# Kernel optimization log

Measured on AMD Instinct MI355X. Metric: run time of the kernel, lower is better.

The kernel has to match this reference:

```python
import jax, jax.numpy as jnp
import numpy as np
from jax import lax

LB, UB = 0.0, 0.1
N_ITERS = 32  # fixed-point iterations for water-filling rebalance


def _conv(x, w, b):
    y = lax.conv_general_dilated(x, w, (1, 1), ((1, 1), (1, 1)),
                                 dimension_numbers=("NCHW", "OIHW", "NCHW"))
    return y + b[None, :, None, None]


def _maxpool2(x):
    return lax.reduce_window(x, -jnp.inf, lax.max, (1, 1, 2, 2), (1, 1, 2, 2), "VALID")


def _linear(x, w, b):
    return x @ w.T + b


def _gru(x_num, W_ih, W_hh, b_ih, b_hh):
    # x_num: [B, S, N]; torch GRU gate order r, z, n
    B = x_num.shape[0]
    H = W_hh.shape[1]
    xs = jnp.swapaxes(x_num, 0, 1)  # [S, B, N]

    def step(h, x_t):
        gi = x_t @ W_ih.T + b_ih            # [B, 3H]
        gh = h @ W_hh.T + b_hh              # [B, 3H]
        i_r, i_z, i_n = jnp.split(gi, 3, axis=-1)
        h_r, h_z, h_n = jnp.split(gh, 3, axis=-1)
        r = jax.nn.sigmoid(i_r + h_r)
        z = jax.nn.sigmoid(i_z + h_z)
        n = jnp.tanh(i_n + r * h_n)
        h_new = (1.0 - z) * n + z * h
        return h_new, None

    h0 = jnp.zeros((B, H), dtype=x_num.dtype)
    h_last, _ = lax.scan(step, h0, xs)
    return h_last


def _rebalance_one(w):
    # vectorized fixed-point version of the per-sample while-loop water-filling
    def body(carry, _):
        old, wc = carry
        leftover = jnp.sum(old - wc)
        mask = wc != UB
        s = jnp.sum(jnp.where(mask, wc, 0.0))
        gift = jnp.where(mask & (s > 0), leftover * wc / jnp.where(s > 0, s, 1.0), 0.0)
        new_old = wc + gift
        new_wc = jnp.clip(new_old, LB, UB)
        return (new_old, new_wc), None

    init = (w, jnp.clip(w, LB, UB))
    (_, wc), _ = lax.scan(body, init, None, length=N_ITERS)
    return wc


def setup_inputs() -> dict:
    key = jax.random.key(0)
    ks = jax.random.split(key, 16)
    B, S, N, H_IMG, W_IMG, HID = 16, 60, 50, 64, 60, 128
    fc_in = 64 * (H_IMG // 4) * (W_IMG // 4)  # 15360
    sc = 0.05
    return {
        "x_num": jax.random.normal(ks[0], (B, S, N), jnp.float32),
        "x_img": jax.random.uniform(ks[1], (B, N, H_IMG, W_IMG), jnp.float32),
        "conv1_w": jax.random.normal(ks[2], (32, 1, 3, 3), jnp.float32) * sc,
        "conv1_b": jnp.zeros((32,), jnp.float32),
        "conv2_w": jax.random.normal(ks[3], (64, 32, 3, 3), jnp.float32) * sc,
        "conv2_b": jnp.zeros((64,), jnp.float32),
        "fc1_w": jax.random.normal(ks[4], (64, fc_in), jnp.float32) * 0.01,
        "fc1_b": jnp.zeros((64,), jnp.float32),
        "fc_binary_w": jax.random.normal(ks[5], (1, 64), jnp.float32) * sc,
        "fc_binary_b": jnp.zeros((1,), jnp.float32),
        "fc2_w": jax.random.normal(ks[6], (128, 64), jnp.float32) * sc,
        "fc2_b": jnp.zeros((128,), jnp.float32),
        "W_ih": jax.random.normal(ks[7], (3 * HID, N), jnp.float32) * sc,
        "W_hh": jax.random.normal(ks[8], (3 * HID, HID), jnp.float32) * sc,
        "b_ih": jnp.zeros((3 * HID,), jnp.float32),
        "b_hh": jnp.zeros((3 * HID,), jnp.float32),
        "gru_fc_w": jax.random.normal(ks[9], (N, HID), jnp.float32) * sc,
        "gru_fc_b": jnp.zeros((N,), jnp.float32),
        "fusion_w": jax.random.normal(ks[10], (64, N + 128), jnp.float32) * sc,
        "fusion_b": jnp.zeros((64,), jnp.float32),
        "final_w": jax.random.normal(ks[11], (N, 64), jnp.float32) * sc,
        "final_b": jnp.zeros((N,), jnp.float32),
    }


def reference(x_num, x_img, conv1_w, conv1_b, conv2_w, conv2_b, fc1_w, fc1_b,
              fc_binary_w, fc_binary_b, fc2_w, fc2_b, W_ih, W_hh, b_ih, b_hh,
              gru_fc_w, gru_fc_b, fusion_w, fusion_b, final_w, final_b):
    B, S, N = x_num.shape
    # GRU branch: last hidden -> Linear -> [B, N]
    h_last = _gru(x_num, W_ih, W_hh, b_ih, b_hh)
    numerical_features = _linear(h_last, gru_fc_w, gru_fc_b)

    # CNN branch on per-stock chart images
    xi = x_img.reshape(B * N, 1, x_img.shape[2], x_img.shape[3])
    h = _maxpool2(jax.nn.relu(_conv(xi, conv1_w, conv1_b)))
    h = _maxpool2(jax.nn.relu(_conv(h, conv2_w, conv2_b)))
    h = h.reshape(B * N, -1)
    feats = jax.nn.relu(_linear(h, fc1_w, fc1_b))
    binary_pred = jax.nn.sigmoid(_linear(feats, fc_binary_w, fc_binary_b))
    cnn_features = _linear(feats, fc2_w, fc2_b).reshape(B, N, -1).mean(axis=1)

    fused = jax.nn.relu(_linear(jnp.concatenate([numerical_features, cnn_features], axis=1), fusion_w, fusion_b))
    w = jax.nn.softmax(_linear(fused, final_w, final_b), axis=1)
    portfolio_weights = jax.vmap(_rebalance_one)(w)
    return portfolio_weights, binary_pred.reshape(B, N)
```

## Files before the change

### kernel.cpp

```cpp
#include <hip/hip_runtime.h>
#include <hip/hip_bf16.h>

typedef unsigned short ushort_t;
typedef short short8_t __attribute__((ext_vector_type(8)));
typedef float f32x4 __attribute__((ext_vector_type(4)));
typedef float f32x16 __attribute__((ext_vector_type(16)));
typedef ushort_t us4_t __attribute__((ext_vector_type(4)));

#define NBATCH 16
#define SEQ    60
#define NSTK   50
#define HID    128
#define G3     384
#define NIMG   800
#define IH     64
#define IW     60
#define P1H    32
#define P1W    30
#define P2C    64
#define FCIN   15360

#define OFF_WHHF   0u
#define OFF_WPREP  24576u
#define OFF_WFC1   33792u
#define OFF_GI     525312u
#define OFF_HLAST  893952u
#define OFF_POOL2  896000u
#define OFF_FC2O   7040000u
#define OFF_PART   7142400u
#define WS_FLOATS  7961600u

#define E_WHH  49152
#define E_WPR  18432
#define E_FC1  983040
#define E_TOT  (E_WHH + E_WPR + E_FC1)

struct __align__(16) ConvS {
    ushort_t pool1t[18][4][32][8];
    union {
        float    imgp[35][60];
        ushort_t pool2s[64][120];
    } u;
};
struct __align__(16) GruS {
    float    gh[16 * 388];
    ushort_t hb[16 * 136];
};
#define SMEM_BYTES 52224

__device__ __forceinline__ float fast_sig(float x) {
    const float e = __expf(-x);
    return __builtin_amdgcn_rcpf(1.f + e);
}
__device__ __forceinline__ float fast_tanh(float x) {
    const float xc = fmaxf(fminf(x, 15.f), -15.f);
    const float e = __expf(2.f * xc);
    return (e - 1.f) * __builtin_amdgcn_rcpf(e + 1.f);
}

__global__ __launch_bounds__(384) void k_pre(const float* __restrict__ xnum,
                                             const float* __restrict__ wih,
                                             const float* __restrict__ bih,
                                             const float* __restrict__ whh,
                                             const float* __restrict__ c2w,
                                             const float* __restrict__ fc1w,
                                             float* __restrict__ GI,
                                             ushort_t* __restrict__ whhf,
                                             ushort_t* __restrict__ wprep,
                                             ushort_t* __restrict__ wfc1)
{
    const int bid = blockIdx.x;
    if (bid < 960) {
        const int s = bid >> 4, b = bid & 15;
        const int j = threadIdx.x;
        const float* xr = xnum + (size_t)(b * SEQ + s) * NSTK;
        const float* wr = wih + (size_t)j * NSTK;
        float a = bih[j];
        #pragma unroll 10
        for (int k = 0; k < NSTK; ++k) a = fmaf(xr[k], wr[k], a);
        GI[((size_t)s * 16 + b) * G3 + j] = a;
        return;
    }
    const int idx = (bid - 960) * 384 + threadIdx.x;
    if (idx < E_WHH) {
        const int e = idx;
        const int i = e & 7, l = (e >> 3) & 63, ksj = e >> 9;
        const int ks = ksj & 3, jt = ksj >> 2;
        const int j = jt * 16 + (l & 15);
        const int k = ks * 32 + ((l >> 4) << 3) + i;
        __hip_bfloat16 hv = __float2bfloat16(whh[j * HID + k]);
        whhf[e] = *(ushort_t*)&hv;
    } else if (idx < E_WHH + E_WPR) {
        const int e = idx - E_WHH;
        const int i = e & 7, l = (e >> 3) & 63, rest = e >> 9;
        const int ks = rest & 1, mt = rest >> 1;
        const int tap = mt % 9, mm = mt / 9;
        const int oc = mm * 32 + (l & 31);
        const int ic = ks * 16 + ((l >> 5) << 3) + i;
        __hip_bfloat16 hv = __float2bfloat16(c2w[((size_t)oc * 32 + ic) * 9 + tap]);
        wprep[e] = *(ushort_t*)&hv;
    } else if (idx < E_TOT) {
        const int e = idx - (E_WHH + E_WPR);
        const int i = e & 7, l = (e >> 3) & 63, rest = e >> 9;
        const int n = rest & 3, T = rest >> 2;
        const int oc = n * 16 + (l & 15);
        const int k = T * 32 + ((l >> 4) << 3) + i;
        __hip_bfloat16 hv = __float2bfloat16(fc1w[(size_t)oc * FCIN + k]);
        wfc1[e] = *(ushort_t*)&hv;
    }
}

__global__ __launch_bounds__(512, 3) void k_mega(const float* __restrict__ x_img,
                                                 const float* __restrict__ c1w,
                                                 const float* __restrict__ c1b,
                                                 const float* __restrict__ c2b,
                                                 const ushort_t* __restrict__ wprep,
                                                 const float* __restrict__ GI,
                                                 const ushort_t* __restrict__ whhf,
                                                 const float* __restrict__ bhh,
                                                 ushort_t* __restrict__ pool2,
                                                 float* __restrict__ hlast)
{
    extern __shared__ char smraw[];
    const int tid = threadIdx.x;
    const int bid = blockIdx.x;

    if (bid == 0) {
        GruS* g = (GruS*)smraw;
        const int w = tid >> 6, l = tid & 63;
        const int arow = l & 15, kq = l >> 4;
        short8_t wfr[3][4];
        #pragma unroll
        for (int jj = 0; jj < 3; ++jj)
            #pragma unroll
            for (int ks = 0; ks < 4; ++ks)
                wfr[jj][ks] = *(const short8_t*)&whhf[((((w * 3 + jj) * 4 + ks) * 64 + l) * 8)];

        const int b = tid >> 5, hh0 = (tid & 31) * 4;
        const f32x4 bhr = *(const f32x4*)&bhh[hh0];
        const f32x4 bhz = *(const f32x4*)&bhh[128 + hh0];
        const f32x4 bhn = *(const f32x4*)&bhh[256 + hh0];
        float h0 = 0.f, h1 = 0.f, h2 = 0.f, h3 = 0.f;
        for (int i = tid; i < 1088; i += 512) ((unsigned int*)g->hb)[i] = 0u;
        const float* gi0 = GI + b * G3 + hh0;
        f32x4 cr = *(const f32x4*)(gi0);
        f32x4 cz = *(const f32x4*)(gi0 + 128);
        f32x4 cn = *(const f32x4*)(gi0 + 256);
        __syncthreads();

        for (int s = 0; s < SEQ; ++s) {
            const int sn = (s + 1 < SEQ) ? s + 1 : s;
            const float* gnx = GI + ((size_t)sn * 16 + b) * G3 + hh0;
            const f32x4 nr = *(const f32x4*)(gnx);
            const f32x4 nz = *(const f32x4*)(gnx + 128);
            const f32x4 nn = *(const f32x4*)(gnx + 256);

            #pragma unroll
            for (int jj = 0; jj < 3; ++jj) {
                f32x4 a = {0.f, 0.f, 0.f, 0.f};
                #pragma unroll
                for (int ks = 0; ks < 4; ++ks) {
                    short8_t af = *(const short8_t*)&g->hb[arow * 136 + ks * 32 + kq * 8];
                    a = __builtin_amdgcn_mfma_f32_16x16x32_bf16(af, wfr[jj][ks], a, 0, 0, 0);
                }
                const int jt = w * 3 + jj;
                #pragma unroll
                for (int r = 0; r < 4; ++r)
                    g->gh[(kq * 4 + r) * 388 + jt * 16 + arow] = a[r];
            }
            __syncthreads();

            const f32x4 gr = *(const f32x4*)&g->gh[b * 388 + hh0];
            const f32x4 gz = *(const f32x4*)&g->gh[b * 388 + 128 + hh0];
            const f32x4 gn = *(const f32x4*)&g->gh[b * 388 + 256 + hh0];
            float hv0, hv1, hv2, hv3;
            {
                const float r0 = fast_sig(cr[0] + gr[0] + bhr[0]);
                const float z0 = fast_sig(cz[0] + gz[0] + bhz[0]);
                const float n0 = fast_tanh(cn[0] + r0 * (gn[0] + bhn[0]));
                hv0 = (1.f - z0) * n0 + z0 * h0;
                const float r1 = fast_sig(cr[1] + gr[1] + bhr[1]);
                const float z1 = fast_sig(cz[1] + gz[1] + bhz[1]);
                const float n1 = fast_tanh(cn[1] + r1 * (gn[1] + bhn[1]));
                hv1 = (1.f - z1) * n1 + z1 * h1;
                const float r2 = fast_sig(cr[2] + gr[2] + bhr[2]);
                const float z2 = fast_sig(cz[2] + gz[2] + bhz[2]);
                const float n2 = fast_tanh(cn[2] + r2 * (gn[2] + bhn[2]));
                hv2 = (1.f - z2) * n2 + z2 * h2;
                const float r3 = fast_sig(cr[3] + gr[3] + bhr[3]);
                const float z3 = fast_sig(cz[3] + gz[3] + bhz[3]);
                const float n3 = fast_tanh(cn[3] + r3 * (gn[3] + bhn[3]));
                hv3 = (1.f - z3) * n3 + z3 * h3;
            }
            h0 = hv0; h1 = hv1; h2 = hv2; h3 = hv3;
            us4_t hp;
            { __hip_bfloat16 t0 = __float2bfloat16(h0); hp[0] = *(ushort_t*)&t0; }
            { __hip_bfloat16 t1 = __float2bfloat16(h1); hp[1] = *(ushort_t*)&t1; }
            { __hip_bfloat16 t2 = __float2bfloat16(h2); hp[2] = *(ushort_t*)&t2; }
            { __hip_bfloat16 t3 = __float2bfloat16(h3); hp[3] = *(ushort_t*)&t3; }
            *(us4_t*)&g->hb[b * 136 + hh0] = hp;
            cr = nr; cz = nz; cn = nn;
            __syncthreads();
        }
        f32x4 ho = {h0, h1, h2, h3};
        *(f32x4*)&hlast[b * HID + hh0] = ho;
        return;
    }

    ConvS* c = (ConvS*)smraw;
    const int img  = (bid - 1) >> 1;
    const int half = (bid - 1) & 1;
    const float* xim = x_img + (size_t)img * (IH * IW);
    const int rowbase = 29 * half;

    {
        const short8_t z = {0, 0, 0, 0, 0, 0, 0, 0};
        const int zrow = half ? 17 : 0;
        if (tid < 128) {
            const int cg = tid >> 5, xs = tid & 31;
            *(short8_t*)&c->pool1t[zrow][cg][xs][0] = z;
        } else if (tid < 272) {
            const int q = tid - 128;
            const int ly = q / 8, cg = (q >> 1) & 3, xs = (q & 1) * 31;
            *(short8_t*)&c->pool1t[ly][cg][xs][0] = z;
        }
    }
    {
        const f32x4* src = (const f32x4*)(xim + rowbase * IW);
        f32x4* dst = (f32x4*)c->u.imgp;
        for (int i = tid; i < 525; i += 512) dst[i] = src[i];
    }
    __syncthreads();

    if (tid < 510) {
        const int gj = tid / 30, px = tid - gj * 30;
        const int g = half * 15 + gj;
        const int ly = gj + 1 - half;
        float patch[4][4];
        #pragma unroll
        for (int yy = 0; yy < 4; ++yy) {
            const int giy = 2 * g - 1 + yy;
            const int liy = giy - rowbase;
            #pragma unroll
            for (int xx = 0; xx < 4; ++xx) {
                const int ix = 2 * px - 1 + xx;
                patch[yy][xx] = (giy >= 0 && giy < IH && ix >= 0 && ix < IW)
                                    ? c->u.imgp[liy][ix] : 0.f;
            }
        }
        #pragma unroll
        for (int cg = 0; cg < 4; ++cg) {
            short8_t outv;
            #pragma unroll
            for (int ch8 = 0; ch8 < 8; ++ch8) {
                const int ch = cg * 8 + ch8;
                float wr[9];
                #pragma unroll
                for (int q = 0; q < 9; ++q) wr[q] = c1w[ch * 9 + q];
                const float bia = c1b[ch];
                float best = 0.f;
                #pragma unroll
                for (int dy = 0; dy < 2; ++dy)
                    #pragma unroll
                    for (int dx = 0; dx < 2; ++dx) {
                        float sv = 0.f;
                        #pragma unroll
                        for (int ky = 0; ky < 3; ++ky)
                            #pragma unroll
                            for (int kx = 0; kx < 3; ++kx)
                                sv = fmaf(patch[dy + ky][dx + kx], wr[ky * 3 + kx], sv);
                        best = fmaxf(best, sv + bia);
                    }
                __hip_bfloat16 hv = __float2bfloat16(best);
                outv[ch8] = *(short*)&hv;
            }
            *(short8_t*)&c->pool1t[ly][cg][px + 1][0] = outv;
        }
    }
    __syncthreads();

    {
        const int w  = tid >> 6, l = tid & 63;
        const int m  = w & 1;
        const int hi = l >> 5;
        const int col = l & 31;

        short8_t af[9][2];
        #pragma unroll
        for (int tap = 0; tap < 9; ++tap)
            #pragma unroll
            for (int ks = 0; ks < 2; ++ks)
                af[tap][ks] = *(const short8_t*)&wprep[(((m * 9 + tap) * 2 + ks) * 64 + l) * 8];
        float bia[16];
        #pragma unroll
        for (int r = 0; r < 16; ++r)
            bia[r] = c2b[m * 32 + (r & 3) + 8 * (r >> 2) + 4 * hi];

        const bool wr = ((col & 1) == 0) && (col < 30);
        const int px = col >> 1;

        #pragma unroll
        for (int yy = 0; yy < 2; ++yy) {
            const int ypl = (w >> 1) + yy * 4;
            f32x16 a0, a1;
            #pragma unroll
            for (int r = 0; r < 16; ++r) { a0[r] = 0.f; a1[r] = 0.f; }
            #pragma unroll
            for (int ro = 0; ro < 4; ++ro) {
                const int ly = 2 * ypl + ro;
                short8_t bf[3][2];
                #pragma unroll
                for (int kx = 0; kx < 3; ++kx)
                    #pragma unroll
                    for (int ks = 0; ks < 2; ++ks)
                        bf[kx][ks] = *(const short8_t*)&c->pool1t[ly][ks * 2 + hi][kx + col][0];
                if (ro < 3) {
                    #pragma unroll
                    for (int kx = 0; kx < 3; ++kx)
                        #pragma unroll
                        for (int ks = 0; ks < 2; ++ks)
                            a0 = __builtin_amdgcn_mfma_f32_32x32x16_bf16(af[ro * 3 + kx][ks], bf[kx][ks], a0, 0, 0, 0);
                }
                if (ro >= 1) {
                    #pragma unroll
                    for (int kx = 0; kx < 3; ++kx)
                        #pragma unroll
                        for (int ks = 0; ks < 2; ++ks)
                            a1 = __builtin_amdgcn_mfma_f32_32x32x16_bf16(af[(ro - 1) * 3 + kx][ks], bf[kx][ks], a1, 0, 0, 0);
                }
            }
            #pragma unroll
            for (int r = 0; r < 16; ++r) {
                float v = fmaxf(a0[r], a1[r]);
                v = fmaxf(v, __shfl_xor(v, 1, 64));
                v = fmaxf(v + bia[r], 0.f);
                if (wr) {
                    const int oc = m * 32 + (r & 3) + 8 * (r >> 2) + 4 * hi;
                    __hip_bfloat16 hv = __float2bfloat16(v);
                    c->u.pool2s[oc][ypl * 15 + px] = *(ushort_t*)&hv;
                }
            }
        }
        __syncthreads();
        {
            int4* dst = (int4*)(pool2 + (size_t)img * FCIN);
            const int4* src = (const int4*)c->u.pool2s;
            #pragma unroll
            for (int jj = 0; jj < 2; ++jj) {
                const int i = tid + jj * 512;
                if (i < 960) {
                    const int oc = i / 15, cc = i - oc * 15;
                    dst[oc * 30 + half * 15 + cc] = src[i];
                }
            }
        }
    }
}

__global__ __launch_bounds__(256) void k_fc1(const ushort_t* __restrict__ pool2,
                                             const ushort_t* __restrict__ wfc1,
                                             float* __restrict__ part)
{
    const int mt = blockIdx.x >> 4;
    const int ks = blockIdx.x & 15;
    const int n = threadIdx.x >> 6, l = threadIdx.x & 63;
    const int arow = l & 15, kq = l >> 4;
    const int img16 = mt * 16;
    const ushort_t* Ab = pool2 + (size_t)(img16 + arow) * FCIN + ks * 960 + kq * 8;
    const ushort_t* Bb = wfc1 + ((size_t)(ks * 30 * 4 + n) * 64 + l) * 8;
    f32x4 acc0 = {0.f, 0.f, 0.f, 0.f}, acc1 = {0.f, 0.f, 0.f, 0.f};
    #pragma unroll 5
    for (int t = 0; t < 30; t += 2) {
        const short8_t aA = *(const short8_t*)(Ab + (size_t)t * 32);
        const short8_t bA = *(const short8_t*)(Bb + (size_t)t * 2048);
        const short8_t aB = *(const short8_t*)(Ab + (size_t)(t + 1) * 32);
        const short8_t bB = *(const short8_t*)(Bb + (size_t)(t + 1) * 2048);
        acc0 = __builtin_amdgcn_mfma_f32_16x16x32_bf16(aA, bA, acc0, 0, 0, 0);
        acc1 = __builtin_amdgcn_mfma_f32_16x16x32_bf16(aB, bB, acc1, 0, 0, 0);
    }
    float* dst = &part[((size_t)ks * NIMG + img16 + kq * 4) * 64 + n * 16 + arow];
    #pragma unroll
    for (int r = 0; r < 4; ++r)
        dst[(size_t)r * 64] = acc0[r] + acc1[r];
}

__device__ __forceinline__ float wave_sum(float v) {
    #pragma unroll
    for (int o = 32; o > 0; o >>= 1) v += __shfl_xor(v, o, 64);
    return v;
}
__device__ __forceinline__ float wave_max(float v) {
    #pragma unroll
    for (int o = 32; o > 0; o >>= 1) v = fmaxf(v, __shfl_xor(v, o, 64));
    return v;
}

__global__ __launch_bounds__(512) void k_post(const float* __restrict__ part,
                                              const float* __restrict__ fc1b,
                                              const float* __restrict__ fbw,
                                              const float* __restrict__ fbb,
                                              const float* __restrict__ fc2w,
                                              const float* __restrict__ fc2b,
                                              float* __restrict__ out,
                                              float* __restrict__ fc2o)
{
    const int t = threadIdx.x;
    const int im8 = t >> 6;
    const int tl = t & 63;
    const int img = blockIdx.x * 8 + im8;
    float s = fc1b[tl];
    #pragma unroll
    for (int ks = 0; ks < 16; ++ks) s += part[((size_t)ks * NIMG + img) * 64 + tl];
    const float f = fmaxf(s, 0.f);
    __shared__ float flc[8][64];
    flc[im8][tl] = f;
    const float bs = wave_sum(f * fbw[tl]);
    if (tl == 0) out[800 + img] = 1.f / (1.f + expf(-(bs + fbb[0])));
    __syncthreads();
    #pragma unroll
    for (int q = 0; q < 2; ++q) {
        const int j = tl + q * 64;
        float a2 = fc2b[j];
        #pragma unroll 8
        for (int k = 0; k < 64; ++k) a2 = fmaf(flc[im8][k], fc2w[j * 64 + k], a2);
        fc2o[(size_t)img * 128 + j] = a2;
    }
}

__global__ __launch_bounds__(64) void k_final(const float* __restrict__ hlast,
                                              const float* __restrict__ fc2o,
                                              const float* __restrict__ gw,
                                              const float* __restrict__ gb,
                                              const float* __restrict__ fw,
                                              const float* __restrict__ fb,
                                              const float* __restrict__ finw,
                                              const float* __restrict__ finb,
                                              float* __restrict__ out)
{
    const int b = blockIdx.x, t = threadIdx.x;
    __shared__ float cf[128], nf[64], fu[64];
    #pragma unroll
    for (int jj = 0; jj < 2; ++jj) {
        const int j = t + jj * 64;
        float s = 0.f;
        for (int n = 0; n < NSTK; ++n) s += fc2o[(size_t)(b * NSTK + n) * 128 + j];
        cf[j] = s * (1.0f / 50.0f);
    }
    float s = 0.f;
    if (t < NSTK) {
        s = gb[t];
        for (int k = 0; k < HID; ++k) s = fmaf(hlast[b * HID + k], gw[t * HID + k], s);
    }
    nf[t] = (t < NSTK) ? s : 0.f;
    __syncthreads();
    float f = fb[t];
    for (int k = 0; k < NSTK; ++k) f = fmaf(nf[k], fw[t * 178 + k], f);
    for (int k = 0; k < 128; ++k) f = fmaf(cf[k], fw[t * 178 + 50 + k], f);
    fu[t] = fmaxf(f, 0.f);
    __syncthreads();
    float L = -3.4e38f;
    if (t < NSTK) {
        L = finb[t];
        for (int k = 0; k < 64; ++k) L = fmaf(fu[k], finw[t * 64 + k], L);
    }
    const float m = wave_max(L);
    const float e = (t < NSTK) ? expf(L - m) : 0.f;
    const float se = wave_sum(e);
    const float wv = e / se;
    float old = wv;
    float wc = fminf(fmaxf(wv, 0.f), 0.1f);
    for (int it = 0; it < 32; ++it) {
        const float leftover = wave_sum(old - wc);
        const bool mask = (wc != 0.1f);
        const float ssum = wave_sum(mask ? wc : 0.f);
        const float gift = (mask && ssum > 0.f) ? leftover * wc / ssum : 0.f;
        old = wc + gift;
        wc = fminf(fmaxf(old, 0.f), 0.1f);
    }
    if (t < NSTK) out[b * NSTK + t] = wc;
}

extern "C" void kernel_launch(void* const* d_in, const int* in_sizes, int n_in,
                              void* d_out, int out_size, void* d_ws, size_t ws_size,
                              hipStream_t stream)
{
    const float* x_num = (const float*)d_in[0];
    const float* x_img = (const float*)d_in[1];
    const float* c1w  = (const float*)d_in[2];
    const float* c1b  = (const float*)d_in[3];
    const float* c2w  = (const float*)d_in[4];
    const float* c2b  = (const float*)d_in[5];
    const float* fc1w = (const float*)d_in[6];
    const float* fc1b = (const float*)d_in[7];
    const float* fbw  = (const float*)d_in[8];
    const float* fbb  = (const float*)d_in[9];
    const float* fc2w = (const float*)d_in[10];
    const float* fc2b = (const float*)d_in[11];
    const float* wih  = (const float*)d_in[12];
    const float* whh  = (const float*)d_in[13];
    const float* bih  = (const float*)d_in[14];
    const float* bhh  = (const float*)d_in[15];
    const float* gw   = (const float*)d_in[16];
    const float* gb   = (const float*)d_in[17];
    const float* fw   = (const float*)d_in[18];
    const float* fb   = (const float*)d_in[19];
    const float* finw = (const float*)d_in[20];
    const float* finb = (const float*)d_in[21];
    float* out = (float*)d_out;
    float* ws  = (float*)d_ws;
    if (ws_size < (size_t)WS_FLOATS * 4) return;

    ushort_t* whhf  = (ushort_t*)(ws + OFF_WHHF);
    ushort_t* wprep = (ushort_t*)(ws + OFF_WPREP);
    ushort_t* wfc1  = (ushort_t*)(ws + OFF_WFC1);
    float* GI       = ws + OFF_GI;
    float* hlast    = ws + OFF_HLAST;
    ushort_t* pool2 = (ushort_t*)(ws + OFF_POOL2);
    float* fc2o     = ws + OFF_FC2O;
    float* part     = ws + OFF_PART;

    (void)hipFuncSetAttribute(reinterpret_cast<const void*>(k_mega),
                              hipFuncAttributeMaxDynamicSharedMemorySize, SMEM_BYTES);

    k_pre   <<<960 + 2736, 384, 0, stream>>>(x_num, wih, bih, whh, c2w, fc1w,
                                             GI, whhf, wprep, wfc1);
    k_mega  <<<2 * NIMG + 1, 512, SMEM_BYTES, stream>>>(x_img, c1w, c1b, c2b, wprep,
                                                        GI, whhf, bhh, pool2, hlast);
    k_fc1   <<<50 * 16, 256, 0, stream>>>(pool2, wfc1, part);
    k_post  <<<100, 512, 0, stream>>>(part, fc1b, fbw, fbb, fc2w, fc2b, out, fc2o);
    k_final <<<NBATCH, 64, 0, stream>>>(hlast, fc2o, gw, gb, fw, fb, finw, finb, out);
}
```

Measured before the change: 148.7 us.

## Compute conv1 in packed fp16 and switch conv2 MFMA to fp16

Conv1 now runs in packed half2 arithmetic. Pairs of channels are computed together, with fp16 weights and biases pre-packed by the prep kernel, instead of scalar fp32 FMAs that reloaded weights from global memory. The pool1 tile and the conv2 weights are stored as fp16 and fed to the f16 MFMA instead of bf16. The fc1 loop unroll is raised from 5 to 10. This cuts conv1 ALU work but accumulates in fp16, which risks overflow or lost precision.

```diff
diff --git a/kernel.cpp b/kernel.cpp
--- a/kernel.cpp
+++ b/kernel.cpp
@@ -1,8 +1,11 @@
 #include <hip/hip_runtime.h>
 #include <hip/hip_bf16.h>
+#include <hip/hip_fp16.h>
 
 typedef unsigned short ushort_t;
 typedef short short8_t __attribute__((ext_vector_type(8)));
+typedef _Float16 half8_t __attribute__((ext_vector_type(8)));
+typedef _Float16 h2 __attribute__((ext_vector_type(2)));
 typedef float f32x4 __attribute__((ext_vector_type(4)));
 typedef float f32x16 __attribute__((ext_vector_type(16)));
 typedef ushort_t us4_t __attribute__((ext_vector_type(4)));
@@ -28,12 +31,14 @@
 #define OFF_POOL2  896000u
 #define OFF_FC2O   7040000u
 #define OFF_PART   7142400u
-#define WS_FLOATS  7961600u
+#define OFF_W1H    7961600u
+#define WS_FLOATS  7961760u
 
 #define E_WHH  49152
 #define E_WPR  18432
 #define E_FC1  983040
-#define E_TOT  (E_WHH + E_WPR + E_FC1)
+#define E_W1H  160
+#define E_TOT  (E_WHH + E_WPR + E_FC1 + E_W1H)
 
 struct __align__(16) ConvS {
     ushort_t pool1t[18][4][32][8];
@@ -57,6 +62,12 @@
     const float e = __expf(2.f * xc);
     return (e - 1.f) * __builtin_amdgcn_rcpf(e + 1.f);
 }
+__device__ __forceinline__ h2 hmax2v(h2 a, h2 b) {
+    h2 r;
+    r[0] = a[0] > b[0] ? a[0] : b[0];
+    r[1] = a[1] > b[1] ? a[1] : b[1];
+    return r;
+}
 
 __global__ __launch_bounds__(384) void k_pre(const float* __restrict__ xnum,
                                              const float* __restrict__ wih,
@@ -64,10 +75,13 @@
                                              const float* __restrict__ whh,
                                              const float* __restrict__ c2w,
                                              const float* __restrict__ fc1w,
+                                             const float* __restrict__ c1w,
+                                             const float* __restrict__ c1b,
                                              float* __restrict__ GI,
                                              ushort_t* __restrict__ whhf,
                                              ushort_t* __restrict__ wprep,
-                                             ushort_t* __restrict__ wfc1)
+                                             ushort_t* __restrict__ wfc1,
+                                             unsigned int* __restrict__ w1h)
 {
     const int bid = blockIdx.x;
     if (bid < 960) {
@@ -97,9 +111,9 @@
         const int tap = mt % 9, mm = mt / 9;
         const int oc = mm * 32 + (l & 31);
         const int ic = ks * 16 + ((l >> 5) << 3) + i;
-        __hip_bfloat16 hv = __float2bfloat16(c2w[((size_t)oc * 32 + ic) * 9 + tap]);
-        wprep[e] = *(ushort_t*)&hv;
-    } else if (idx < E_TOT) {
+        const _Float16 hv = (_Float16)c2w[((size_t)oc * 32 + ic) * 9 + tap];
+        wprep[e] = *(const ushort_t*)&hv;
+    } else if (idx < E_WHH + E_WPR + E_FC1) {
         const int e = idx - (E_WHH + E_WPR);
         const int i = e & 7, l = (e >> 3) & 63, rest = e >> 9;
         const int n = rest & 3, T = rest >> 2;
@@ -107,12 +121,26 @@
         const int k = T * 32 + ((l >> 4) << 3) + i;
         __hip_bfloat16 hv = __float2bfloat16(fc1w[(size_t)oc * FCIN + k]);
         wfc1[e] = *(ushort_t*)&hv;
+    } else if (idx < E_TOT) {
+        const int e = idx - (E_WHH + E_WPR + E_FC1);
+        if (e < 144) {
+            const int p = e / 9, tap = e - p * 9;
+            const int ch0 = (p >> 2) * 8 + (p & 3) * 2;
+            const _Float16 lo = (_Float16)c1w[ch0 * 9 + tap];
+            const _Float16 hi = (_Float16)c1w[(ch0 + 1) * 9 + tap];
+            w1h[p * 9 + tap] = ((unsigned)*(const ushort_t*)&hi << 16) | *(const ushort_t*)&lo;
+        } else {
+            const int p = e - 144;
+            const int ch0 = (p >> 2) * 8 + (p & 3) * 2;
+            const _Float16 lo = (_Float16)c1b[ch0];
+            const _Float16 hi = (_Float16)c1b[ch0 + 1];
+            w1h[144 + p] = ((unsigned)*(const ushort_t*)&hi << 16) | *(const ushort_t*)&lo;
+        }
     }
 }
 
 __global__ __launch_bounds__(512, 3) void k_mega(const float* __restrict__ x_img,
-                                                 const float* __restrict__ c1w,
-                                                 const float* __restrict__ c1b,
+                                                 const unsigned int* __restrict__ w1h,
                                                  const float* __restrict__ c2b,
                                                  const ushort_t* __restrict__ wprep,
                                                  const float* __restrict__ GI,
@@ -140,7 +168,7 @@
         const f32x4 bhr = *(const f32x4*)&bhh[hh0];
         const f32x4 bhz = *(const f32x4*)&bhh[128 + hh0];
         const f32x4 bhn = *(const f32x4*)&bhh[256 + hh0];
-        float h0 = 0.f, h1 = 0.f, h2 = 0.f, h3 = 0.f;
+        float h0 = 0.f, h1 = 0.f, h2v = 0.f, h3 = 0.f;
         for (int i = tid; i < 1088; i += 512) ((unsigned int*)g->hb)[i] = 0u;
         const float* gi0 = GI + b * G3 + hh0;
         f32x4 cr = *(const f32x4*)(gi0);
@@ -186,23 +214,23 @@
                 const float r2 = fast_sig(cr[2] + gr[2] + bhr[2]);
                 const float z2 = fast_sig(cz[2] + gz[2] + bhz[2]);
                 const float n2 = fast_tanh(cn[2] + r2 * (gn[2] + bhn[2]));
-                hv2 = (1.f - z2) * n2 + z2 * h2;
+                hv2 = (1.f - z2) * n2 + z2 * h2v;
                 const float r3 = fast_sig(cr[3] + gr[3] + bhr[3]);
                 const float z3 = fast_sig(cz[3] + gz[3] + bhz[3]);
                 const float n3 = fast_tanh(cn[3] + r3 * (gn[3] + bhn[3]));
                 hv3 = (1.f - z3) * n3 + z3 * h3;
             }
-            h0 = hv0; h1 = hv1; h2 = hv2; h3 = hv3;
+            h0 = hv0; h1 = hv1; h2v = hv2; h3 = hv3;
             us4_t hp;
-            { __hip_bfloat16 t0 = __float2bfloat16(h0); hp[0] = *(ushort_t*)&t0; }
-            { __hip_bfloat16 t1 = __float2bfloat16(h1); hp[1] = *(ushort_t*)&t1; }
-            { __hip_bfloat16 t2 = __float2bfloat16(h2); hp[2] = *(ushort_t*)&t2; }
-            { __hip_bfloat16 t3 = __float2bfloat16(h3); hp[3] = *(ushort_t*)&t3; }
+            { __hip_bfloat16 t0 = __float2bfloat16(h0);  hp[0] = *(ushort_t*)&t0; }
+            { __hip_bfloat16 t1 = __float2bfloat16(h1);  hp[1] = *(ushort_t*)&t1; }
+            { __hip_bfloat16 t2 = __float2bfloat16(h2v); hp[2] = *(ushort_t*)&t2; }
+            { __hip_bfloat16 t3 = __float2bfloat16(h3);  hp[3] = *(ushort_t*)&t3; }
             *(us4_t*)&g->hb[b * 136 + hh0] = hp;
             cr = nr; cz = nz; cn = nn;
             __syncthreads();
         }
-        f32x4 ho = {h0, h1, h2, h3};
+        f32x4 ho = {h0, h1, h2v, h3};
         *(f32x4*)&hlast[b * HID + hh0] = ho;
         return;
     }
@@ -236,7 +264,8 @@
         const int gj = tid / 30, px = tid - gj * 30;
         const int g = half * 15 + gj;
         const int ly = gj + 1 - half;
-        float patch[4][4];
+        const h2 z2 = {(_Float16)0.f, (_Float16)0.f};
+        h2 patch2[4][4];
         #pragma unroll
         for (int yy = 0; yy < 4; ++yy) {
             const int giy = 2 * g - 1 + yy;
@@ -244,37 +273,43 @@
             #pragma unroll
             for (int xx = 0; xx < 4; ++xx) {
                 const int ix = 2 * px - 1 + xx;
-                patch[yy][xx] = (giy >= 0 && giy < IH && ix >= 0 && ix < IW)
+                const float v = (giy >= 0 && giy < IH && ix >= 0 && ix < IW)
                                     ? c->u.imgp[liy][ix] : 0.f;
+                const _Float16 vh = (_Float16)v;
+                h2 p2; p2[0] = vh; p2[1] = vh;
+                patch2[yy][xx] = p2;
             }
         }
         #pragma unroll
         for (int cg = 0; cg < 4; ++cg) {
-            short8_t outv;
-            #pragma unroll
-            for (int ch8 = 0; ch8 < 8; ++ch8) {
-                const int ch = cg * 8 + ch8;
-                float wr[9];
+            unsigned int ov[4];
+            #pragma unroll
+            for (int pr = 0; pr < 4; ++pr) {
+                const int p = cg * 4 + pr;
+                h2 wv[9];
                 #pragma unroll
-                for (int q = 0; q < 9; ++q) wr[q] = c1w[ch * 9 + q];
-                const float bia = c1b[ch];
-                float best = 0.f;
+                for (int t = 0; t < 9; ++t) {
+                    const unsigned int wu = w1h[p * 9 + t];
+                    wv[t] = *(const h2*)&wu;
+                }
+                h2 a00 = z2, a01 = z2, a10 = z2, a11 = z2;
                 #pragma unroll
-                for (int dy = 0; dy < 2; ++dy)
+                for (int ky = 0; ky < 3; ++ky)
                     #pragma unroll
-                    for (int dx = 0; dx < 2; ++dx) {
-                        float sv = 0.f;
-                        #pragma unroll
-                        for (int ky = 0; ky < 3; ++ky)
-                            #pragma unroll
-                            for (int kx = 0; kx < 3; ++kx)
-                                sv = fmaf(patch[dy + ky][dx + kx], wr[ky * 3 + kx], sv);
-                        best = fmaxf(best, sv + bia);
+                    for (int kx = 0; kx < 3; ++kx) {
+                        const h2 wt = wv[ky * 3 + kx];
+                        a00 = wt * patch2[ky][kx]     + a00;
+                        a01 = wt * patch2[ky][kx + 1] + a01;
+                        a10 = wt * patch2[ky + 1][kx] + a10;
+                        a11 = wt * patch2[ky + 1][kx + 1] + a11;
                     }
-                __hip_bfloat16 hv = __float2bfloat16(best);
-                outv[ch8] = *(short*)&hv;
-            }
-            *(short8_t*)&c->pool1t[ly][cg][px + 1][0] = outv;
+                const unsigned int bu = w1h[144 + p];
+                const h2 bia2 = *(const h2*)&bu;
+                h2 m = hmax2v(hmax2v(a00, a01), hmax2v(a10, a11));
+                h2 r = hmax2v(m + bia2, z2);
+                ov[pr] = *(unsigned int*)&r;
+            }
+            *(uint4*)&c->pool1t[ly][cg][px + 1][0] = *(uint4*)ov;
         }
     }
     __syncthreads();
@@ -285,12 +320,12 @@
         const int hi = l >> 5;
         const int col = l & 31;
 
-        short8_t af[9][2];
+        half8_t af[9][2];
         #pragma unroll
         for (int tap = 0; tap < 9; ++tap)
             #pragma unroll
             for (int ks = 0; ks < 2; ++ks)
-                af[tap][ks] = *(const short8_t*)&wprep[(((m * 9 + tap) * 2 + ks) * 64 + l) * 8];
+                af[tap][ks] = *(const half8_t*)&wprep[(((m * 9 + tap) * 2 + ks) * 64 + l) * 8];
         float bia[16];
         #pragma unroll
         for (int r = 0; r < 16; ++r)
@@ -308,25 +343,25 @@
             #pragma unroll
             for (int ro = 0; ro < 4; ++ro) {
                 const int ly = 2 * ypl + ro;
-                short8_t bf[3][2];
+                half8_t bf[3][2];
                 #pragma unroll
                 for (int kx = 0; kx < 3; ++kx)
                     #pragma unroll
                     for (int ks = 0; ks < 2; ++ks)
-                        bf[kx][ks] = *(const short8_t*)&c->pool1t[ly][ks * 2 + hi][kx + col][0];
+                        bf[kx][ks] = *(const half8_t*)&c->pool1t[ly][ks * 2 + hi][kx + col][0];
                 if (ro < 3) {
                     #pragma unroll
                     for (int kx = 0; kx < 3; ++kx)
                         #pragma unroll
                         for (int ks = 0; ks < 2; ++ks)
-                            a0 = __builtin_amdgcn_mfma_f32_32x32x16_bf16(af[ro * 3 + kx][ks], bf[kx][ks], a0, 0, 0, 0);
+                            a0 = __builtin_amdgcn_mfma_f32_32x32x16_f16(af[ro * 3 + kx][ks], bf[kx][ks], a0, 0, 0, 0);
                 }
                 if (ro >= 1) {
                     #pragma unroll
                     for (int kx = 0; kx < 3; ++kx)
                         #pragma unroll
                         for (int ks = 0; ks < 2; ++ks)
-                            a1 = __builtin_amdgcn_mfma_f32_32x32x16_bf16(af[(ro - 1) * 3 + kx][ks], bf[kx][ks], a1, 0, 0, 0);
+                            a1 = __builtin_amdgcn_mfma_f32_32x32x16_f16(af[(ro - 1) * 3 + kx][ks], bf[kx][ks], a1, 0, 0, 0);
                 }
             }
             #pragma unroll
@@ -369,7 +404,7 @@
     const ushort_t* Ab = pool2 + (size_t)(img16 + arow) * FCIN + ks * 960 + kq * 8;
     const ushort_t* Bb = wfc1 + ((size_t)(ks * 30 * 4 + n) * 64 + l) * 8;
     f32x4 acc0 = {0.f, 0.f, 0.f, 0.f}, acc1 = {0.f, 0.f, 0.f, 0.f};
-    #pragma unroll 5
+    #pragma unroll 10
     for (int t = 0; t < 30; t += 2) {
         const short8_t aA = *(const short8_t*)(Ab + (size_t)t * 32);
         const short8_t bA = *(const short8_t*)(Bb + (size_t)t * 2048);
@@ -518,13 +553,14 @@
     ushort_t* pool2 = (ushort_t*)(ws + OFF_POOL2);
     float* fc2o     = ws + OFF_FC2O;
     float* part     = ws + OFF_PART;
+    unsigned int* w1h = (unsigned int*)(ws + OFF_W1H);
 
     (void)hipFuncSetAttribute(reinterpret_cast<const void*>(k_mega),
                               hipFuncAttributeMaxDynamicSharedMemorySize, SMEM_BYTES);
 
-    k_pre   <<<960 + 2736, 384, 0, stream>>>(x_num, wih, bih, whh, c2w, fc1w,
-                                             GI, whhf, wprep, wfc1);
-    k_mega  <<<2 * NIMG + 1, 512, SMEM_BYTES, stream>>>(x_img, c1w, c1b, c2b, wprep,
+    k_pre   <<<960 + 2737, 384, 0, stream>>>(x_num, wih, bih, whh, c2w, fc1w, c1w, c1b,
+                                             GI, whhf, wprep, wfc1, w1h);
+    k_mega  <<<2 * NIMG + 1, 512, SMEM_BYTES, stream>>>(x_img, w1h, c2b, wprep,
                                                         GI, whhf, bhh, pool2, hlast);
     k_fc1   <<<50 * 16, 256, 0, stream>>>(pool2, wfc1, part);
     k_post  <<<100, 512, 0, stream>>>(part, fc1b, fbw, fbb, fc2w, fc2b, out, fc2o);
```

Result: no change. 146.1 us (-1.7%).
